# Optimization experiments

Hardware: AMD Instinct MI355X
Metric: run time of the kernel (lower is better)

Reference implementation:

```python
import jax, jax.numpy as jnp
import numpy as np

V = 50000   # vocab_size
E = 300     # embed_dim (GRU input size)
H = 256     # hidden_dim
R = 2048    # number of replies
L0 = 128    # original content length
LR = 64     # max reply length (padded)

def setup_inputs() -> dict:
    key = jax.random.key(0)
    ks = jax.random.split(key, 20)
    s = 0.05
    inp = {
        "original_tokens": jax.random.randint(ks[0], (L0,), 0, V),
        "reply_tokens":    jax.random.randint(ks[1], (R, LR), 0, V),
        "reply_lengths":   jax.random.randint(ks[2], (R,), 1, LR + 1),
        "label":           jax.random.uniform(ks[3], (1,), dtype=jnp.float32),
        # learned params
        "embed": jax.random.normal(ks[4], (V, E), dtype=jnp.float32) * s,
        # bi-GRU forward direction (PyTorch layout: gates [r, z, n] stacked)
        "Wih_f": jax.random.normal(ks[5], (3 * H, E), dtype=jnp.float32) * s,
        "Whh_f": jax.random.normal(ks[6], (3 * H, H), dtype=jnp.float32) * s,
        "bih_f": jax.random.normal(ks[7], (3 * H,), dtype=jnp.float32) * s,
        "bhh_f": jax.random.normal(ks[8], (3 * H,), dtype=jnp.float32) * s,
        # bi-GRU reverse direction
        "Wih_b": jax.random.normal(ks[9], (3 * H, E), dtype=jnp.float32) * s,
        "Whh_b": jax.random.normal(ks[10], (3 * H, H), dtype=jnp.float32) * s,
        "bih_b": jax.random.normal(ks[11], (3 * H,), dtype=jnp.float32) * s,
        "bhh_b": jax.random.normal(ks[12], (3 * H,), dtype=jnp.float32) * s,
        # self.linear : 2H -> H
        "Wl": jax.random.normal(ks[13], (H, 2 * H), dtype=jnp.float32) * s,
        "bl": jax.random.normal(ks[14], (H,), dtype=jnp.float32) * s,
        # self.output_linear : H -> 1 (batch_size = 1)
        "Wo": jax.random.normal(ks[15], (1, H), dtype=jnp.float32) * s,
        "bo": jax.random.normal(ks[16], (1,), dtype=jnp.float32) * s,
    }
    return inp


def _gru_dir(x, Wih, Whh, bih, bhh):
    """Single-direction GRU over x: (S, E) -> (ys: (S, H), hT: (H,)).
    PyTorch gate math: r,z,n with n = tanh(gi_n + r * gh_n)."""
    def step(h, xt):
        gi = Wih @ xt + bih            # (3H,)
        gh = Whh @ h + bhh             # (3H,)
        r = jax.nn.sigmoid(gi[:H] + gh[:H])
        z = jax.nn.sigmoid(gi[H:2 * H] + gh[H:2 * H])
        n = jnp.tanh(gi[2 * H:] + r * gh[2 * H:])
        h_new = (1.0 - z) * n + z * h
        return h_new, h_new
    h0 = jnp.zeros((H,), dtype=x.dtype)
    hT, ys = jax.lax.scan(step, h0, x)
    return ys, hT


def reference(original_tokens, reply_tokens, reply_lengths, label,
              embed, Wih_f, Whh_f, bih_f, bhh_f,
              Wih_b, Whh_b, bih_b, bhh_b, Wl, bl, Wo, bo):
    # per-event embedding + sum pooling (batched replacement of Python loop)
    orig = embed[original_tokens].sum(axis=0)                      # (E,)
    mask = (jnp.arange(LR)[None, :] < reply_lengths[:, None]).astype(embed.dtype)
    rep = jnp.einsum('rle,rl->re', embed[reply_tokens], mask)      # (R, E)
    X = jnp.concatenate([orig[None, :], rep], axis=0)              # (S, E), S = R+1

    # bidirectional GRU (batch dim is 1, squeezed)
    ys_f, h_f = _gru_dir(X, Wih_f, Whh_f, bih_f, bhh_f)            # (S, H), (H,)
    ys_b, h_b = _gru_dir(X[::-1], Wih_b, Whh_b, bih_b, bhh_b)
    ys_b = ys_b[::-1]                                              # (S, H)

    out2 = jnp.concatenate([ys_f, ys_b], axis=-1)                  # (S, 2H)
    output = out2 @ Wl.T + bl                                      # (S, H)

    # hidden = sum over directions of final hidden states
    hsum = h_f + h_b                                               # (H,)

    # dot-product attention: query = hsum, keys = values = output
    scores = output @ hsum                                         # (S,)
    w = jax.nn.softmax(scores)                                     # attention dist
    ctx = w @ output                                               # (H,)

    result = jax.nn.sigmoid(ctx @ Wo.T + bo)                       # (1,)
    loss = (label - result) ** 2                                   # (1,)
    return (output[:, None, :], loss, result)                      # output: (S,1,H)
```

## Files before the change

kernel.cpp:

```cpp
#include <hip/hip_runtime.h>
#include <cstdint>
#include <cstddef>

#define NV 50000
#define NE 300
#define NH 256
#define NR 2048
#define NL0 128
#define NLR 64
#define NS 2049
#define G3 768

static constexpr size_t alignUp(size_t x, size_t a) { return (x + a - 1) / a * a; }
static constexpr size_t OFF_CTX    = 0;
static constexpr size_t OFF_SCORES = OFF_CTX + 1024;
static constexpr size_t OFF_X      = alignUp(OFF_SCORES + (size_t)NS * 4, 256);
static constexpr size_t OFF_GI_F   = alignUp(OFF_X + (size_t)NS * NE * 4, 256);
static constexpr size_t OFF_GI_B   = alignUp(OFF_GI_F + (size_t)NS * G3 * 4, 256);
static constexpr size_t OFF_OUT2   = alignUp(OFF_GI_B + (size_t)NS * G3 * 4, 256);

typedef _Float16 half2t __attribute__((ext_vector_type(2)));

#if __has_builtin(__builtin_amdgcn_fdot2)
__device__ __forceinline__ float fdot2(half2t a, half2t b, float c) {
    return __builtin_amdgcn_fdot2(a, b, c, false);
}
#else
__device__ __forceinline__ float fdot2(half2t a, half2t b, float c) {
    return c + (float)a[0] * (float)b[0] + (float)a[1] * (float)b[1];
}
#endif

__global__ __launch_bounds__(320) void embed_sum_kernel(
    const int* __restrict__ otok, const int* __restrict__ rtok,
    const int* __restrict__ rlen, const float* __restrict__ embed,
    float* __restrict__ X)
{
    const int b = blockIdx.x;
    const int e = threadIdx.x;
    if (e >= NE) return;
    float acc = 0.f;
    if (b == 0) {
        for (int t = 0; t < NL0; ++t) {
            int tok = otok[t];
            acc += embed[(size_t)tok * NE + e];
        }
    } else {
        const int r = b - 1;
        const int L = rlen[r];
        const int* tr = rtok + (size_t)r * NLR;
        for (int t = 0; t < L; ++t) {
            int tok = tr[t];
            acc += embed[(size_t)tok * NE + e];
        }
    }
    X[(size_t)b * NE + e] = acc;
}

__global__ __launch_bounds__(256) void gemm_abt(
    const float* __restrict__ A, const float* __restrict__ B,
    const float* __restrict__ bias, float* __restrict__ C,
    int M, int N, int K, int ldc)
{
    __shared__ float As[16][65];
    __shared__ float Bs[16][65];
    const int bm = blockIdx.x * 64, bn = blockIdx.y * 64;
    const int tid = threadIdx.x;
    const int tx = tid & 15, ty = tid >> 4;
    float acc[4][4] = {};
    for (int k0 = 0; k0 < K; k0 += 16) {
        #pragma unroll
        for (int i = 0; i < 4; ++i) {
            int l = tid + 256 * i;
            int mm = l >> 4, kk = l & 15;
            int gm = bm + mm, gk = k0 + kk;
            As[kk][mm] = (gm < M && gk < K) ? A[(size_t)gm * K + gk] : 0.f;
            int gn = bn + mm;
            Bs[kk][mm] = (gk < K) ? B[(size_t)gn * K + gk] : 0.f;
        }
        __syncthreads();
        #pragma unroll
        for (int kk = 0; kk < 16; ++kk) {
            float a0 = As[kk][ty], a1 = As[kk][ty+16], a2 = As[kk][ty+32], a3 = As[kk][ty+48];
            float b0 = Bs[kk][tx], b1 = Bs[kk][tx+16], b2 = Bs[kk][tx+32], b3 = Bs[kk][tx+48];
            acc[0][0] += a0*b0; acc[0][1] += a0*b1; acc[0][2] += a0*b2; acc[0][3] += a0*b3;
            acc[1][0] += a1*b0; acc[1][1] += a1*b1; acc[1][2] += a1*b2; acc[1][3] += a1*b3;
            acc[2][0] += a2*b0; acc[2][1] += a2*b1; acc[2][2] += a2*b2; acc[2][3] += a2*b3;
            acc[3][0] += a3*b0; acc[3][1] += a3*b1; acc[3][2] += a3*b2; acc[3][3] += a3*b3;
        }
        __syncthreads();
    }
    #pragma unroll
    for (int i = 0; i < 4; ++i) {
        int gm = bm + ty + 16 * i;
        if (gm >= M) continue;
        #pragma unroll
        for (int j = 0; j < 4; ++j) {
            int gn = bn + tx + 16 * j;
            C[(size_t)gm * ldc + gn] = acc[i][j] + bias[gn];
        }
    }
}

__device__ __forceinline__ float dpp_add_xor1(float x) {
    int v = __builtin_amdgcn_update_dpp(0, __float_as_int(x), 0xB1, 0xF, 0xF, true);
    return x + __int_as_float(v);
}

__global__ __launch_bounds__(512) void gru_kernel(
    const float* __restrict__ Whh_f, const float* __restrict__ bhh_f,
    const float* __restrict__ Whh_b, const float* __restrict__ bhh_b,
    const float* __restrict__ gi_f, const float* __restrict__ gi_b,
    float* __restrict__ out2)
{
    const int dir  = blockIdx.x;
    const int tid  = threadIdx.x;
    const int e    = tid >> 1;
    const int hsel = tid & 1;

    const float* __restrict__ Whh = dir ? Whh_b : Whh_f;
    const float* __restrict__ bhh = dir ? bhh_b : bhh_f;
    const float* __restrict__ gi  = dir ? gi_b  : gi_f;

    __shared__ __align__(16) _Float16 hl16[2][NH];
    __shared__ float hf32[2][NH];

    if (tid < NH) { hl16[0][tid] = (_Float16)0.f; hf32[0][tid] = 0.f; }

    half2t wr[64], wz[64], wn[64];
    {
        const float2* r0 = (const float2*)(Whh + (size_t)e * NH            + hsel * 128);
        const float2* r1 = (const float2*)(Whh + (size_t)(NH + e) * NH     + hsel * 128);
        const float2* r2 = (const float2*)(Whh + (size_t)(2 * NH + e) * NH + hsel * 128);
        #pragma unroll
        for (int c = 0; c < 64; ++c) {
            float2 a = r0[c], b = r1[c], d = r2[c];
            wr[c] = half2t{(_Float16)a.x, (_Float16)a.y};
            wz[c] = half2t{(_Float16)b.x, (_Float16)b.y};
            wn[c] = half2t{(_Float16)d.x, (_Float16)d.y};
        }
    }
    const float bhr = bhh[e], bhz = bhh[NH + e], bhn = bhh[2 * NH + e];

    float gir, giz, gin;
    {
        const float* g0 = gi + (size_t)(dir ? NS - 1 : 0) * G3 + e;
        gir = g0[0]; giz = g0[NH]; gin = g0[2 * NH];
    }
    __syncthreads();

    for (int t = 0; t < NS; ++t) {
        const int p = t & 1;
        const int s = dir ? (NS - 1 - t) : t;

        float girN = 0.f, gizN = 0.f, ginN = 0.f;
        if (t < NS - 1) {
            const float* gn = gi + (size_t)(dir ? (NS - 2 - t) : (t + 1)) * G3 + e;
            girN = gn[0]; gizN = gn[NH]; ginN = gn[2 * NH];
        }

        const float hprev = hf32[p][e];
        const uint4* hq = (const uint4*)&hl16[p][hsel * 128];

        float ar0 = 0.f, ar1 = 0.f, az0 = 0.f, az1 = 0.f, an0 = 0.f, an1 = 0.f;
        #pragma unroll
        for (int c = 0; c < 16; ++c) {
            uint4 q = hq[c];
            half2t h0 = __builtin_bit_cast(half2t, q.x);
            half2t h1 = __builtin_bit_cast(half2t, q.y);
            half2t h2 = __builtin_bit_cast(half2t, q.z);
            half2t h3 = __builtin_bit_cast(half2t, q.w);
            ar0 = fdot2(wr[c*4+0], h0, ar0); az0 = fdot2(wz[c*4+0], h0, az0); an0 = fdot2(wn[c*4+0], h0, an0);
            ar1 = fdot2(wr[c*4+1], h1, ar1); az1 = fdot2(wz[c*4+1], h1, az1); an1 = fdot2(wn[c*4+1], h1, an1);
            ar0 = fdot2(wr[c*4+2], h2, ar0); az0 = fdot2(wz[c*4+2], h2, az0); an0 = fdot2(wn[c*4+2], h2, an0);
            ar1 = fdot2(wr[c*4+3], h3, ar1); az1 = fdot2(wz[c*4+3], h3, az1); an1 = fdot2(wn[c*4+3], h3, an1);
        }
        float ar = ar0 + ar1, az = az0 + az1, an = an0 + an1;
        ar = dpp_add_xor1(ar);
        az = dpp_add_xor1(az);
        an = dpp_add_xor1(an);

        const float r  = 1.f / (1.f + __expf(-(gir + ar + bhr)));
        const float z  = 1.f / (1.f + __expf(-(giz + az + bhz)));
        const float n  = tanhf(gin + r * (an + bhn));
        const float hn = (1.f - z) * n + z * hprev;

        if (hsel == 0) {
            hf32[p ^ 1][e] = hn;
            hl16[p ^ 1][e] = (_Float16)hn;
            out2[(size_t)s * (2 * NH) + dir * NH + e] = hn;
        }
        gir = girN; giz = gizN; gin = ginN;
        __syncthreads();
    }
}

__global__ __launch_bounds__(256) void scores_kernel(
    const float* __restrict__ outp, const float* __restrict__ out2,
    float* __restrict__ scores)
{
    const int s = blockIdx.x, m = threadIdx.x;
    float hs = out2[(size_t)(NS - 1) * (2 * NH) + m] + out2[NH + m];
    float v = outp[(size_t)s * NH + m] * hs;
    #pragma unroll
    for (int o = 32; o > 0; o >>= 1) v += __shfl_down(v, o);
    __shared__ float p[4];
    if ((m & 63) == 0) p[m >> 6] = v;
    __syncthreads();
    if (m == 0) scores[s] = p[0] + p[1] + p[2] + p[3];
}

__global__ __launch_bounds__(1024) void softmax_kernel(float* __restrict__ sc)
{
    const int tid = threadIdx.x;
    __shared__ float red[16];
    float x0 = (tid < NS) ? sc[tid] : -3.0e38f;
    float x1 = (tid + 1024 < NS) ? sc[tid + 1024] : -3.0e38f;
    float mx = fmaxf(x0, x1);
    #pragma unroll
    for (int o = 32; o > 0; o >>= 1) mx = fmaxf(mx, __shfl_xor(mx, o));
    if ((tid & 63) == 0) red[tid >> 6] = mx;
    __syncthreads();
    if (tid == 0) {
        float m = red[0];
        for (int i = 1; i < 16; ++i) m = fmaxf(m, red[i]);
        red[0] = m;
    }
    __syncthreads();
    const float gmax = red[0];
    float e0 = (tid < NS) ? __expf(x0 - gmax) : 0.f;
    float e1 = (tid + 1024 < NS) ? __expf(x1 - gmax) : 0.f;
    float sm = e0 + e1;
    #pragma unroll
    for (int o = 32; o > 0; o >>= 1) sm += __shfl_xor(sm, o);
    __syncthreads();
    if ((tid & 63) == 0) red[tid >> 6] = sm;
    __syncthreads();
    if (tid == 0) {
        float su = 0.f;
        for (int i = 0; i < 16; ++i) su += red[i];
        red[1] = 1.f / su;
    }
    __syncthreads();
    const float inv = red[1];
    if (tid < NS) sc[tid] = e0 * inv;
    if (tid + 1024 < NS) sc[tid + 1024] = e1 * inv;
}

__global__ __launch_bounds__(256) void ctx_kernel(
    const float* __restrict__ outp, const float* __restrict__ w,
    float* __restrict__ ctx)
{
    const int m = threadIdx.x;
    const int s0 = blockIdx.x * 128;
    const int s1 = min(s0 + 128, NS);
    float acc = 0.f;
    for (int s = s0; s < s1; ++s) acc += w[s] * outp[(size_t)s * NH + m];
    atomicAdd(&ctx[m], acc);
}

__global__ __launch_bounds__(256) void final_kernel(
    const float* __restrict__ ctx, const float* __restrict__ Wo,
    const float* __restrict__ bo, const float* __restrict__ label,
    float* __restrict__ dout)
{
    const int m = threadIdx.x;
    float v = ctx[m] * Wo[m];
    #pragma unroll
    for (int o = 32; o > 0; o >>= 1) v += __shfl_down(v, o);
    __shared__ float p[4];
    if ((m & 63) == 0) p[m >> 6] = v;
    __syncthreads();
    if (m == 0) {
        float x = p[0] + p[1] + p[2] + p[3] + bo[0];
        float result = 1.f / (1.f + __expf(-x));
        float d = label[0] - result;
        dout[(size_t)NS * NH]     = d * d;
        dout[(size_t)NS * NH + 1] = result;
    }
}

extern "C" void kernel_launch(void* const* d_in, const int* in_sizes, int n_in,
                              void* d_out, int out_size, void* d_ws, size_t ws_size,
                              hipStream_t stream)
{
    const int*   otok  = (const int*)d_in[0];
    const int*   rtok  = (const int*)d_in[1];
    const int*   rlen  = (const int*)d_in[2];
    const float* label = (const float*)d_in[3];
    const float* embed = (const float*)d_in[4];
    const float* Wih_f = (const float*)d_in[5];
    const float* Whh_f = (const float*)d_in[6];
    const float* bih_f = (const float*)d_in[7];
    const float* bhh_f = (const float*)d_in[8];
    const float* Wih_b = (const float*)d_in[9];
    const float* Whh_b = (const float*)d_in[10];
    const float* bih_b = (const float*)d_in[11];
    const float* bhh_b = (const float*)d_in[12];
    const float* Wl    = (const float*)d_in[13];
    const float* bl    = (const float*)d_in[14];
    const float* Wo    = (const float*)d_in[15];
    const float* bo    = (const float*)d_in[16];

    char* ws = (char*)d_ws;
    float* ctx    = (float*)(ws + OFF_CTX);
    float* scores = (float*)(ws + OFF_SCORES);
    float* X      = (float*)(ws + OFF_X);
    float* gi_f   = (float*)(ws + OFF_GI_F);
    float* gi_b   = (float*)(ws + OFF_GI_B);
    float* out2   = (float*)(ws + OFF_OUT2);
    float* outp   = (float*)d_out;

    hipMemsetAsync(ws + OFF_CTX, 0, 1024, stream);

    embed_sum_kernel<<<NS, 320, 0, stream>>>(otok, rtok, rlen, embed, X);

    gemm_abt<<<dim3(33, 12), 256, 0, stream>>>(X, Wih_f, bih_f, gi_f, NS, G3, NE, G3);
    gemm_abt<<<dim3(33, 12), 256, 0, stream>>>(X, Wih_b, bih_b, gi_b, NS, G3, NE, G3);

    gru_kernel<<<2, 512, 0, stream>>>(Whh_f, bhh_f, Whh_b, bhh_b,
                                      gi_f, gi_b, out2);

    gemm_abt<<<dim3(33, 4), 256, 0, stream>>>(out2, Wl, bl, outp, NS, NH, 2 * NH, NH);

    scores_kernel<<<NS, 256, 0, stream>>>(outp, out2, scores);
    softmax_kernel<<<1, 1024, 0, stream>>>(scores);
    ctx_kernel<<<(NS + 127) / 128, 256, 0, stream>>>(outp, scores, ctx);
    final_kernel<<<1, 256, 0, stream>>>(ctx, Wo, bo, label, (float*)d_out);
}
```

Baseline: 2.867 ms.

## Use MFMA for GRU recurrent matvec with LDS gate exchange

Replaces the per-thread fdot2 recurrent matvec in the sequential GRU kernel with MFMA 16x16x32 f16 instructions. Each wave holds fp16 weight tiles in registers and multiplies them by the hidden vector broadcast across the B operand. Results go through shared memory, and then 256 threads apply the gate math. It also keeps h in a register, uses an exp-based tanh, and defers the out2 store by one step to take global writes off the critical path. This adds a second barrier per step and wastes 15 of 16 MFMA columns, trading that for fewer instructions per step on a latency-bound recurrence.

New measurement: 2.946 ms. 2.8% more time.

```diff
diff --git a/kernel.cpp b/kernel.cpp
--- a/kernel.cpp
+++ b/kernel.cpp
@@ -19,17 +19,13 @@
 static constexpr size_t OFF_GI_B   = alignUp(OFF_GI_F + (size_t)NS * G3 * 4, 256);
 static constexpr size_t OFF_OUT2   = alignUp(OFF_GI_B + (size_t)NS * G3 * 4, 256);
 
-typedef _Float16 half2t __attribute__((ext_vector_type(2)));
-
-#if __has_builtin(__builtin_amdgcn_fdot2)
-__device__ __forceinline__ float fdot2(half2t a, half2t b, float c) {
-    return __builtin_amdgcn_fdot2(a, b, c, false);
-}
-#else
-__device__ __forceinline__ float fdot2(half2t a, half2t b, float c) {
-    return c + (float)a[0] * (float)b[0] + (float)a[1] * (float)b[1];
-}
-#endif
+typedef _Float16 f16x8 __attribute__((ext_vector_type(8)));
+typedef float    f32x4 __attribute__((ext_vector_type(4)));
+
+__device__ __forceinline__ float tanh_fast(float x) {
+    float t = __expf(2.f * x);
+    return 1.f - 2.f / (t + 1.f);
+}
 
 __global__ __launch_bounds__(320) void embed_sum_kernel(
     const int* __restrict__ otok, const int* __restrict__ rtok,
@@ -102,11 +98,6 @@
     }
 }
 
-__device__ __forceinline__ float dpp_add_xor1(float x) {
-    int v = __builtin_amdgcn_update_dpp(0, __float_as_int(x), 0xB1, 0xF, 0xF, true);
-    return x + __int_as_float(v);
-}
-
 __global__ __launch_bounds__(512) void gru_kernel(
     const float* __restrict__ Whh_f, const float* __restrict__ bhh_f,
     const float* __restrict__ Whh_b, const float* __restrict__ bhh_b,
@@ -115,35 +106,49 @@
 {
     const int dir  = blockIdx.x;
     const int tid  = threadIdx.x;
-    const int e    = tid >> 1;
-    const int hsel = tid & 1;
+    const int lane = tid & 63;
+    const int wave = tid >> 6;
+    const int lg   = lane >> 4;
+    const int lr   = lane & 15;
 
     const float* __restrict__ Whh = dir ? Whh_b : Whh_f;
     const float* __restrict__ bhh = dir ? bhh_b : bhh_f;
     const float* __restrict__ gi  = dir ? gi_b  : gi_f;
 
     __shared__ __align__(16) _Float16 hl16[2][NH];
-    __shared__ float hf32[2][NH];
-
-    if (tid < NH) { hl16[0][tid] = (_Float16)0.f; hf32[0][tid] = 0.f; }
-
-    half2t wr[64], wz[64], wn[64];
+    __shared__ __align__(16) float    ysh[G3];
+
+    if (tid < NH) hl16[0][tid] = (_Float16)0.f;
+
+    f16x8 wA[6][8];
     {
-        const float2* r0 = (const float2*)(Whh + (size_t)e * NH            + hsel * 128);
-        const float2* r1 = (const float2*)(Whh + (size_t)(NH + e) * NH     + hsel * 128);
-        const float2* r2 = (const float2*)(Whh + (size_t)(2 * NH + e) * NH + hsel * 128);
-        #pragma unroll
-        for (int c = 0; c < 64; ++c) {
-            float2 a = r0[c], b = r1[c], d = r2[c];
-            wr[c] = half2t{(_Float16)a.x, (_Float16)a.y};
-            wz[c] = half2t{(_Float16)b.x, (_Float16)b.y};
-            wn[c] = half2t{(_Float16)d.x, (_Float16)d.y};
-        }
-    }
-    const float bhr = bhh[e], bhz = bhh[NH + e], bhn = bhh[2 * NH + e];
-
-    float gir, giz, gin;
-    {
+        #pragma unroll
+        for (int i = 0; i < 6; ++i) {
+            const float* rowp = Whh + (size_t)((wave * 6 + i) * 16 + lr) * NH + lg * 8;
+            #pragma unroll
+            for (int kt = 0; kt < 8; ++kt) {
+                float4 a = *(const float4*)(rowp + kt * 32);
+                float4 b = *(const float4*)(rowp + kt * 32 + 4);
+                f16x8 w;
+                w[0] = (_Float16)a.x; w[1] = (_Float16)a.y;
+                w[2] = (_Float16)a.z; w[3] = (_Float16)a.w;
+                w[4] = (_Float16)b.x; w[5] = (_Float16)b.y;
+                w[6] = (_Float16)b.z; w[7] = (_Float16)b.w;
+                wA[i][kt] = w;
+                __builtin_amdgcn_sched_barrier(0);
+            }
+        }
+    }
+
+    const bool isGate = (tid < NH);
+    const int  e = tid;
+    float bhr = 0.f, bhz = 0.f, bhn = 0.f;
+    float gir = 0.f, giz = 0.f, gin = 0.f;
+    float hreg = 0.f;
+    float hnPend = 0.f;
+    int   offPend = 0;
+    if (isGate) {
+        bhr = bhh[e]; bhz = bhh[NH + e]; bhn = bhh[2 * NH + e];
         const float* g0 = gi + (size_t)(dir ? NS - 1 : 0) * G3 + e;
         gir = g0[0]; giz = g0[NH]; gin = g0[2 * NH];
     }
@@ -153,46 +158,51 @@
         const int p = t & 1;
         const int s = dir ? (NS - 1 - t) : t;
 
+        if (isGate && t > 0) out2[offPend] = hnPend;
+
         float girN = 0.f, gizN = 0.f, ginN = 0.f;
-        if (t < NS - 1) {
+        if (isGate && t < NS - 1) {
             const float* gn = gi + (size_t)(dir ? (NS - 2 - t) : (t + 1)) * G3 + e;
             girN = gn[0]; gizN = gn[NH]; ginN = gn[2 * NH];
         }
 
-        const float hprev = hf32[p][e];
-        const uint4* hq = (const uint4*)&hl16[p][hsel * 128];
-
-        float ar0 = 0.f, ar1 = 0.f, az0 = 0.f, az1 = 0.f, an0 = 0.f, an1 = 0.f;
-        #pragma unroll
-        for (int c = 0; c < 16; ++c) {
-            uint4 q = hq[c];
-            half2t h0 = __builtin_bit_cast(half2t, q.x);
-            half2t h1 = __builtin_bit_cast(half2t, q.y);
-            half2t h2 = __builtin_bit_cast(half2t, q.z);
-            half2t h3 = __builtin_bit_cast(half2t, q.w);
-            ar0 = fdot2(wr[c*4+0], h0, ar0); az0 = fdot2(wz[c*4+0], h0, az0); an0 = fdot2(wn[c*4+0], h0, an0);
-            ar1 = fdot2(wr[c*4+1], h1, ar1); az1 = fdot2(wz[c*4+1], h1, az1); an1 = fdot2(wn[c*4+1], h1, an1);
-            ar0 = fdot2(wr[c*4+2], h2, ar0); az0 = fdot2(wz[c*4+2], h2, az0); an0 = fdot2(wn[c*4+2], h2, an0);
-            ar1 = fdot2(wr[c*4+3], h3, ar1); az1 = fdot2(wz[c*4+3], h3, az1); an1 = fdot2(wn[c*4+3], h3, an1);
-        }
-        float ar = ar0 + ar1, az = az0 + az1, an = an0 + an1;
-        ar = dpp_add_xor1(ar);
-        az = dpp_add_xor1(az);
-        an = dpp_add_xor1(an);
-
-        const float r  = 1.f / (1.f + __expf(-(gir + ar + bhr)));
-        const float z  = 1.f / (1.f + __expf(-(giz + az + bhz)));
-        const float n  = tanhf(gin + r * (an + bhn));
-        const float hn = (1.f - z) * n + z * hprev;
-
-        if (hsel == 0) {
-            hf32[p ^ 1][e] = hn;
+        const _Float16* hp = &hl16[p][0];
+        #pragma unroll
+        for (int grp = 0; grp < 2; ++grp) {
+            f32x4 a0 = {0.f, 0.f, 0.f, 0.f};
+            f32x4 a1 = {0.f, 0.f, 0.f, 0.f};
+            f32x4 a2 = {0.f, 0.f, 0.f, 0.f};
+            #pragma unroll
+            for (int kt = 0; kt < 8; ++kt) {
+                uint4 u = *(const uint4*)(hp + kt * 32 + lg * 8);
+                f16x8 hb = __builtin_bit_cast(f16x8, u);
+                a0 = __builtin_amdgcn_mfma_f32_16x16x32_f16(wA[grp*3+0][kt], hb, a0, 0, 0, 0);
+                a1 = __builtin_amdgcn_mfma_f32_16x16x32_f16(wA[grp*3+1][kt], hb, a1, 0, 0, 0);
+                a2 = __builtin_amdgcn_mfma_f32_16x16x32_f16(wA[grp*3+2][kt], hb, a2, 0, 0, 0);
+            }
+            if (lr == 0) {
+                *(f32x4*)(&ysh[(wave * 6 + grp * 3 + 0) * 16 + lg * 4]) = a0;
+                *(f32x4*)(&ysh[(wave * 6 + grp * 3 + 1) * 16 + lg * 4]) = a1;
+                *(f32x4*)(&ysh[(wave * 6 + grp * 3 + 2) * 16 + lg * 4]) = a2;
+            }
+        }
+        __syncthreads();
+
+        if (isGate) {
+            const float yr = ysh[e], yz = ysh[NH + e], yn = ysh[2 * NH + e];
+            const float r  = 1.f / (1.f + __expf(-(gir + yr + bhr)));
+            const float z  = 1.f / (1.f + __expf(-(giz + yz + bhz)));
+            const float n  = tanh_fast(gin + r * (yn + bhn));
+            const float hn = (1.f - z) * n + z * hreg;
+            hreg = hn;
             hl16[p ^ 1][e] = (_Float16)hn;
-            out2[(size_t)s * (2 * NH) + dir * NH + e] = hn;
-        }
-        gir = girN; giz = gizN; gin = ginN;
+            hnPend  = hn;
+            offPend = s * (2 * NH) + dir * NH + e;
+            gir = girN; giz = gizN; gin = ginN;
+        }
         __syncthreads();
     }
+    if (isGate) out2[offPend] = hnPend;
 }
 
 __global__ __launch_bounds__(256) void scores_kernel(
```
